# Performance work log

Measured on AMD Instinct MI355X. Metric: run time of the kernel, lower is better.

The kernel has to match this reference:

```python
import jax, jax.numpy as jnp
import numpy as np

# Standard 2D morphsnakes structuring elements (4 line filters), matching the
# repo-level global `filters` used by LSNet2.
_SE = np.zeros((4, 3, 3), dtype=np.float32)
_SE[0, 1, :] = 1.0           # horizontal line
_SE[1, :, 1] = 1.0           # vertical line
_SE[2] = np.eye(3, dtype=np.float32)          # main diagonal
_SE[3] = np.eye(3, dtype=np.float32)[::-1]    # anti-diagonal


def _dilate_stack(x, filts):
    # per-pixel: max over 3x3 window of (zero-padded x + filt), for every filter
    H, W = x.shape
    p = jnp.pad(x, 1)
    m = jnp.full((filts.shape[0], H, W), -jnp.inf, x.dtype)
    for k in range(3):
        for l in range(3):
            m = jnp.maximum(m, p[k:k + H, l:l + W][None] + filts[:, k, l][:, None, None])
    return m  # [F, H, W]


def _erode_stack(x, filts):
    # per-pixel: min over 3x3 window of (zero-padded x - filt) == -max(-(x - filt))
    H, W = x.shape
    p = jnp.pad(x, 1)
    m = jnp.full((filts.shape[0], H, W), jnp.inf, x.dtype)
    for k in range(3):
        for l in range(3):
            m = jnp.minimum(m, p[k:k + H, l:l + W][None] - filts[:, k, l][:, None, None])
    return m  # [F, H, W]


def _dilate_min(x, filts):
    return jnp.min(_dilate_stack(x, filts), axis=0)


def _erode_max(x, filts):
    return jnp.max(_erode_stack(x, filts), axis=0)


def setup_inputs() -> dict:
    key = jax.random.key(0)
    k1, k2 = jax.random.split(key)
    H = W = 2048
    inp = jax.random.uniform(k1, (H, W), dtype=jnp.float32)
    origin = jax.random.uniform(k2, (H, W), dtype=jnp.float32)
    filters = jnp.asarray(_SE)
    return {"input": inp, "origin": origin, "filters": filters}


def reference(input, origin, filters):
    x = input
    # SI o IS smoothing: dilate/min, erode/max, erode/max, dilate/min, dilate/min, erode/max
    x = _dilate_min(x, filters)
    x = _erode_max(x, filters)
    x = _erode_max(x, filters)
    x = _dilate_min(x, filters)
    x = _dilate_min(x, filters)
    x = _erode_max(x, filters)

    # balloon force with v = 1 and a flat ones(3,3) structuring element
    ones_f = jnp.ones((1, 3, 3), x.dtype)
    aux = _dilate_stack(x, ones_f)[0]
    threshold = jnp.percentile(x, 40.0)
    x = jnp.where(origin > threshold, aux, x)

    # Chan-Vese region means and update
    c0 = jnp.sum(origin * (1.0 - x)) / (jnp.sum(1.0 - x) + 1e-8)
    c1 = jnp.sum(origin * x) / (jnp.sum(x) + 1e-8)
    cv = (origin - c1) ** 2 - (origin - c0) ** 2
    x = jnp.where(cv < 0, 1.0, jnp.where(cv > 0, 0.0, x))
    return x
```

## Files before the change

kernel.cpp:

```cpp
#include <hip/hip_runtime.h>

#define HH 2048
#define WW 2048
#define NN (HH*WW)

static constexpr unsigned RANK0 = 1677721u;
static constexpr unsigned KEYLO = 0xB000u;
static constexpr unsigned KEYHI_ = 0xC000u;
static constexpr int NBINS = 4096;
static constexpr int NPART = 2048;

#define TH 32
#define TW 128
#define LR 44
#define LCP 148

static constexpr size_t OFF_CTL    = (size_t)NN * 4;
static constexpr size_t OFF_COARSE = OFF_CTL;
static constexpr size_t OFF_UNDER  = OFF_COARSE + (size_t)NBINS * 4;
static constexpr size_t OFF_OVER   = OFF_UNDER + 4;
static constexpr size_t OFF_MIDA   = OFF_OVER + 4;
static constexpr size_t OFF_MIDB   = OFF_MIDA + 1024;
static constexpr size_t OFF_H2A    = OFF_MIDB + 1024;
static constexpr size_t OFF_H2B    = OFF_H2A + 65536ull * 4;
static constexpr size_t CTL_END    = OFF_H2B + 65536ull * 4;
static constexpr size_t CTL_BYTES  = CTL_END - OFF_CTL;
static constexpr size_t OFF_PART   = CTL_END;

__device__ __forceinline__ float mx3(float a, float b, float c){ return fmaxf(fmaxf(a,b),c); }
__device__ __forceinline__ float mn3(float a, float b, float c){ return fminf(fminf(a,b),c); }

__device__ __forceinline__ unsigned keyf(float x){
  unsigned b = __float_as_uint(x);
  return (b & 0x80000000u) ? ~b : (b | 0x80000000u);
}
__device__ __forceinline__ float keyinv(unsigned k){
  unsigned b = (k & 0x80000000u) ? (k ^ 0x80000000u) : ~k;
  return __uint_as_float(b);
}

__device__ __forceinline__ unsigned excl_scan256(unsigned v, volatile unsigned* tmp, int t){
  int lane = t & 63, wv = t >> 6;
  unsigned inc = v;
  #pragma unroll
  for (int off = 1; off < 64; off <<= 1){
    unsigned u = __shfl_up(inc, off);
    if (lane >= off) inc += u;
  }
  if (lane == 63) tmp[wv] = inc;
  __syncthreads();
  unsigned wo = 0;
  #pragma unroll
  for (int w = 0; w < 4; w++) wo += (w < wv) ? tmp[w] : 0u;
  __syncthreads();
  return wo + inc - v;
}

__device__ __forceinline__ void coarse_rank(const unsigned* __restrict__ gh,
                                            const unsigned* __restrict__ under,
                                            unsigned* cres, volatile unsigned* stmp, int t){
  unsigned bins[16], loc = 0;
  #pragma unroll
  for (int i = 0; i < 16; i++){ bins[i] = gh[t*16 + i]; loc += bins[i]; }
  unsigned run = excl_scan256(loc, stmp, t) + under[0];
  #pragma unroll
  for (int i = 0; i < 16; i++){
    unsigned cc = bins[i];
    if (cc){
      if (RANK0 >= run && RANK0 - run < cc){ cres[0] = KEYLO + (unsigned)(t*16+i); cres[1] = RANK0 - run; }
      if (RANK0+1 >= run && RANK0+1 - run < cc){ cres[2] = KEYLO + (unsigned)(t*16+i); cres[3] = RANK0+1 - run; }
    }
    run += cc;
  }
  __syncthreads();
}

__device__ __forceinline__ void rank256(const unsigned* __restrict__ h, unsigned r,
                                        unsigned* res2, volatile unsigned* stmp, int t){
  unsigned c = h[t];
  unsigned ex = excl_scan256(c, stmp, t);
  if (c && r >= ex && r - ex < c){ res2[0] = (unsigned)t; res2[1] = r - ex; }
  __syncthreads();
}

__device__ __forceinline__ void loadwin6(const float* __restrict__ src, int rowbase,
                                         int cL, int cC, int cR, float w[6]){
  float4 v = *reinterpret_cast<const float4*>(&src[rowbase + cC]);
  w[0] = src[rowbase + cL];
  w[1]=v.x; w[2]=v.y; w[3]=v.z; w[4]=v.w;
  w[5] = src[rowbase + cR];
}

__device__ __forceinline__ void morph4(bool DIL,
    const float pr[6], const float cr[6], const float nr[6], float w[4]){
  #pragma unroll
  for (int i = 0; i < 4; i++){
    if (DIL){
      float Ah = mx3(cr[i],   cr[i+1], cr[i+2]);
      float Av = mx3(pr[i+1], cr[i+1], nr[i+1]);
      float Ad = mx3(pr[i],   cr[i+1], nr[i+2]);
      float Aa = mx3(pr[i+2], cr[i+1], nr[i]);
      float tm = mx3(pr[i], pr[i+1], pr[i+2]);
      float bm = mx3(nr[i], nr[i+1], nr[i+2]);
      float M9 = mx3(tm, Ah, bm);
      w[i] = fmaxf(M9, 1.0f + fminf(fminf(Ah,Av), fminf(Ad,Aa)));
    } else {
      float Bh = mn3(cr[i],   cr[i+1], cr[i+2]);
      float Bv = mn3(pr[i+1], cr[i+1], nr[i+1]);
      float Bd = mn3(pr[i],   cr[i+1], nr[i+2]);
      float Ba = mn3(pr[i+2], cr[i+1], nr[i]);
      float tm = mn3(pr[i], pr[i+1], pr[i+2]);
      float bm = mn3(nr[i], nr[i+1], nr[i+2]);
      float m9 = mn3(tm, Bh, bm);
      w[i] = fminf(m9, fmaxf(fmaxf(Bh,Bv), fmaxf(Bd,Ba)) - 1.0f);
    }
  }
}

__global__ __launch_bounds__(256)
void fused_morph_k(const float* __restrict__ in, float* __restrict__ out,
                   unsigned* __restrict__ gh, unsigned* __restrict__ under,
                   unsigned* __restrict__ over){
  __shared__ float lds[2][LR*LCP];
  const int tilec = blockIdx.x & 15;
  const int tiler = blockIdx.x >> 4;
  const int r0 = tiler*TH, c0 = tilec*TW;

  for (int idx = threadIdx.x; idx < LR*36; idx += 256){
    int lr = idx / 36, g = idx % 36;
    int gr = r0 - 6 + lr, gc = c0 - 8 + 4*g;
    float4 v = make_float4(0.f,0.f,0.f,0.f);
    if ((unsigned)gr < (unsigned)HH && (unsigned)gc < (unsigned)WW)
      v = *reinterpret_cast<const float4*>(in + (size_t)gr*WW + gc);
    *reinterpret_cast<float4*>(&lds[0][lr*LCP + 4*g]) = v;
  }
  __syncthreads();

  const int t = threadIdx.x;
  const int g = t % 36, s = t / 36;
  const bool active = (t < 252);
  const int colC = 4*g;
  const int colL = g ? 4*g - 1 : 0;
  const int colR = (g == 35) ? 143 : 4*g + 4;
  const int gcBase = c0 - 8 + 4*g;
  const bool dilf[6] = {true,false,false,true,true,false};

  #pragma unroll 1
  for (int st = 0; st < 6; st++){
    const float* src = lds[st & 1];
    float*       dst = lds[(st & 1) ^ 1];
    if (active){
      const bool DIL = dilf[st];
      float r8[8][6];
      #pragma unroll
      for (int k = 0; k < 8; k++)
        loadwin6(src, (6*s + k)*LCP, colL, colC, colR, r8[k]);
      #pragma unroll
      for (int k = 0; k < 6; k++){
        float w[4];
        morph4(DIL, r8[k], r8[k+1], r8[k+2], w);
        int gr = r0 - 6 + 6*s + 1 + k;
        if ((unsigned)gr >= (unsigned)HH){
          w[0]=w[1]=w[2]=w[3]=0.f;
        } else {
          #pragma unroll
          for (int i = 0; i < 4; i++)
            if ((unsigned)(gcBase + i) >= (unsigned)WW) w[i] = 0.f;
        }
        *reinterpret_cast<float4*>(&dst[(6*s + 1 + k)*LCP + colC]) =
            make_float4(w[0],w[1],w[2],w[3]);
      }
    }
    __syncthreads();
  }
  unsigned* lh = reinterpret_cast<unsigned*>(&lds[1][0]);
  for (int i = threadIdx.x; i < NBINS; i += 256) lh[i] = 0;
  __syncthreads();

  unsigned uc = 0, oc = 0;
  for (int idx = threadIdx.x; idx < TH*(TW/4); idx += 256){
    int row = idx >> 5, gg = idx & 31;
    float4 v = *reinterpret_cast<const float4*>(&lds[0][(row+6)*LCP + 8 + 4*gg]);
    *reinterpret_cast<float4*>(out + (size_t)(r0+row)*WW + c0 + 4*gg) = v;
    float vv[4] = {v.x, v.y, v.z, v.w};
    #pragma unroll
    for (int i = 0; i < 4; i++){
      unsigned key = keyf(vv[i]);
      unsigned hi = key >> 16;
      if (hi >= KEYLO && hi < KEYHI_) atomicAdd(&lh[hi - KEYLO], 1u);
      else if (hi < KEYLO)            uc++;
      else                            oc++;
    }
  }
  __syncthreads();
  for (int i = threadIdx.x; i < NBINS; i += 256){
    unsigned c = lh[i];
    if (c) atomicAdd(&gh[i], c);
  }
  if (uc) atomicAdd(under, uc);
  if (oc) atomicAdd(over, oc);
}

__global__ __launch_bounds__(256)
void fine2d_k(const float* __restrict__ x,
              const unsigned* __restrict__ coarse, const unsigned* __restrict__ under,
              unsigned* __restrict__ midA, unsigned* __restrict__ midB,
              unsigned* __restrict__ h2A, unsigned* __restrict__ h2B){
  __shared__ unsigned hA[256], hB[256];
  __shared__ unsigned stmp[4], cres[4];
  const int t = threadIdx.x;
  coarse_rank(coarse, under, cres, stmp, t);
  unsigned ha = cres[0], hb = cres[2];
  bool dup = (ha == hb);
  hA[t] = 0; hB[t] = 0;
  __syncthreads();
  const int nItems = NN/4;
  for (int it = blockIdx.x*blockDim.x + t; it < nItems; it += gridDim.x*blockDim.x){
    float4 v = reinterpret_cast<const float4*>(x)[it];
    float vv[4] = {v.x, v.y, v.z, v.w};
    #pragma unroll
    for (int j = 0; j < 4; j++){
      unsigned key = keyf(vv[j]);
      unsigned hi = key >> 16;
      if (hi == ha){ atomicAdd(&hA[(key>>8)&255], 1u); atomicAdd(&h2A[key & 0xFFFFu], 1u); }
      else if (hi == hb){ atomicAdd(&hB[(key>>8)&255], 1u); atomicAdd(&h2B[key & 0xFFFFu], 1u); }
    }
  }
  __syncthreads();
  if (hA[t]) atomicAdd(&midA[t], hA[t]);
  if (!dup && hB[t]) atomicAdd(&midB[t], hB[t]);
}

__device__ __forceinline__ void load6(const float* __restrict__ p, int row, int q, float r[6]){
  if (row < 0 || row >= HH){
    r[0]=r[1]=r[2]=r[3]=r[4]=r[5]=0.f;
    return;
  }
  const float* rp = p + (size_t)row * WW;
  float4 cc = *reinterpret_cast<const float4*>(rp + q);
  r[0] = (q > 0) ? rp[q-1] : 0.f;
  r[1]=cc.x; r[2]=cc.y; r[3]=cc.z; r[4]=cc.w;
  r[5] = (q+4 < WW) ? rp[q+4] : 0.f;
}

__global__ __launch_bounds__(256)
void balloon_k(const float* __restrict__ x, const float* __restrict__ orig,
               float* __restrict__ xb,
               const unsigned* __restrict__ coarse, const unsigned* __restrict__ under,
               const unsigned* __restrict__ midA, const unsigned* __restrict__ midB,
               const unsigned* __restrict__ h2A, const unsigned* __restrict__ h2B,
               double* __restrict__ part){
  __shared__ unsigned stmp[4], cres[4], mresA[2], mresB[2], lresA[2], lresB[2];
  __shared__ double red[4][3];
  const int t = threadIdx.x;

  coarse_rank(coarse, under, cres, stmp, t);
  unsigned ha = cres[0], rA = cres[1], hb = cres[2], rB = cres[3];
  bool dupHi = (ha == hb);
  rank256(midA, rA, mresA, stmp, t);
  rank256(dupHi ? midA : midB, rB, mresB, stmp, t);
  unsigned mA = mresA[0], rA2 = mresA[1], mB = mresB[0], rB2 = mresB[1];
  rank256(h2A + (size_t)mA*256, rA2, lresA, stmp, t);
  rank256((dupHi ? h2A : h2B) + (size_t)mB*256, rB2, lresB, stmp, t);
  unsigned ka = (ha << 16) | (mA << 8) | lresA[0];
  unsigned kb = (hb << 16) | (mB << 8) | lresB[0];
  double va = (double)keyinv(ka), vb = (double)keyinv(kb);
  const double FRAC = 0.4*(double)(NN-1) - (double)RANK0;
  double thr = va + (vb - va) * FRAC;

  double s0 = 0.0, s1 = 0.0, s2 = 0.0;
  const int nItems = NN/4;
  for (int it = blockIdx.x*blockDim.x + t; it < nItems; it += gridDim.x*blockDim.x){
    int i = it >> 9;
    int q = (it & 511) << 2;
    float a[6], b[6], c[6];
    load6(x, i-1, q, a);
    load6(x, i,   q, b);
    load6(x, i+1, q, c);
    float4 og = *reinterpret_cast<const float4*>(orig + (size_t)i*WW + q);
    float ov[4] = {og.x, og.y, og.z, og.w};
    float r[4];
    #pragma unroll
    for (int j = 0; j < 4; j++){
      float M9 = mx3(mx3(a[j],a[j+1],a[j+2]), mx3(b[j],b[j+1],b[j+2]), mx3(c[j],c[j+1],c[j+2]));
      float aux = 1.0f + M9;
      float nx = ((double)ov[j] > thr) ? aux : b[j+1];
      r[j] = nx;
      s0 += (double)ov[j];
      s1 += (double)nx;
      s2 += (double)ov[j] * (double)nx;
    }
    *reinterpret_cast<float4*>(xb + (size_t)i*WW + q) = make_float4(r[0],r[1],r[2],r[3]);
  }
  for (int off = 32; off > 0; off >>= 1){
    s0 += __shfl_down(s0, off);
    s1 += __shfl_down(s1, off);
    s2 += __shfl_down(s2, off);
  }
  int lane = t & 63, wv = t >> 6;
  if (lane == 0){ red[wv][0] = s0; red[wv][1] = s1; red[wv][2] = s2; }
  __syncthreads();
  if (t == 0){
    part[blockIdx.x*3+0] = red[0][0]+red[1][0]+red[2][0]+red[3][0];
    part[blockIdx.x*3+1] = red[0][1]+red[1][1]+red[2][1]+red[3][1];
    part[blockIdx.x*3+2] = red[0][2]+red[1][2]+red[2][2]+red[3][2];
  }
}

__global__ __launch_bounds__(256)
void final_k(const float* __restrict__ orig, const float* __restrict__ xb,
             const double* __restrict__ part, float* __restrict__ out){
  __shared__ double red[4][3];
  __shared__ double cc01[2];
  const int t = threadIdx.x;
  {
    double u0 = 0, u1 = 0, u2 = 0;
    for (int b = t; b < NPART; b += 256){
      u0 += part[b*3+0]; u1 += part[b*3+1]; u2 += part[b*3+2];
    }
    for (int off = 32; off > 0; off >>= 1){
      u0 += __shfl_down(u0, off);
      u1 += __shfl_down(u1, off);
      u2 += __shfl_down(u2, off);
    }
    int lane = t & 63, wv = t >> 6;
    if (lane == 0){ red[wv][0] = u0; red[wv][1] = u1; red[wv][2] = u2; }
    __syncthreads();
    if (t == 0){
      double So = red[0][0]+red[1][0]+red[2][0]+red[3][0];
      double Sx = red[0][1]+red[1][1]+red[2][1]+red[3][1];
      double Sox= red[0][2]+red[1][2]+red[2][2]+red[3][2];
      cc01[0] = (So - Sox) / ((double)NN - Sx + 1e-8);
      cc01[1] = Sox / (Sx + 1e-8);
    }
    __syncthreads();
  }
  double c0 = cc01[0], c1 = cc01[1];
  const int nItems = NN/4;
  for (int it = blockIdx.x*blockDim.x + t; it < nItems; it += gridDim.x*blockDim.x){
    float4 og = reinterpret_cast<const float4*>(orig)[it];
    float4 xv = reinterpret_cast<const float4*>(xb)[it];
    float ov[4] = {og.x, og.y, og.z, og.w};
    float xx[4] = {xv.x, xv.y, xv.z, xv.w};
    float r[4];
    #pragma unroll
    for (int j = 0; j < 4; j++){
      double o = (double)ov[j];
      double d1 = o - c1, d0 = o - c0;
      double cv = d1*d1 - d0*d0;
      r[j] = (cv < 0.0) ? 1.0f : ((cv > 0.0) ? 0.0f : xx[j]);
    }
    reinterpret_cast<float4*>(out)[it] = make_float4(r[0],r[1],r[2],r[3]);
  }
}

extern "C" void kernel_launch(void* const* d_in, const int* in_sizes, int n_in,
                              void* d_out, int out_size, void* d_ws, size_t ws_size,
                              hipStream_t stream) {
  const float* input  = (const float*)d_in[0];
  const float* origin = (const float*)d_in[1];
  float* out = (float*)d_out;

  char* ws = (char*)d_ws;
  float*    bufA   = (float*)ws;
  unsigned* coarse = (unsigned*)(ws + OFF_COARSE);
  unsigned* under  = (unsigned*)(ws + OFF_UNDER);
  unsigned* over   = (unsigned*)(ws + OFF_OVER);
  unsigned* midA   = (unsigned*)(ws + OFF_MIDA);
  unsigned* midB   = (unsigned*)(ws + OFF_MIDB);
  unsigned* h2A    = (unsigned*)(ws + OFF_H2A);
  unsigned* h2B    = (unsigned*)(ws + OFF_H2B);
  double*   part   = (double*)(ws + OFF_PART);

  hipMemsetAsync(ws + OFF_CTL, 0, CTL_BYTES, stream);

  fused_morph_k<<<(HH/TH)*(WW/TW), 256, 0, stream>>>(input, out, coarse, under, over);
  fine2d_k<<<2048, 256, 0, stream>>>(out, coarse, under, midA, midB, h2A, h2B);
  balloon_k<<<2048, 256, 0, stream>>>(out, origin, bufA, coarse, under,
                                      midA, midB, h2A, h2B, part);
  final_k<<<2048, 256, 0, stream>>>(origin, bufA, part, out);
}
```

Baseline: 124.2 us.

## Hoist c0/c1 reduction into single-block kernel, shrink grids, use float4 halo loads

Moves the partial-sum reduction and c0/c1 computation out of every final_k block into a separate one-block kernel that writes the two scalars to workspace, so final_k just reads them. The balloon grid shrinks to 512 blocks (fewer partials) and fine2d to 1024 blocks. The morph stencil loads its left and right halo values with aligned float4 LDS reads instead of scalar reads. This removes redundant reductions across 2048 blocks, at the cost of an extra kernel launch and possibly less parallelism in the resized kernels.

Result: faster. 112.7 us (median of 3 runs) (-9.3%).

```diff
diff --git a/kernel.cpp b/kernel.cpp
--- a/kernel.cpp
+++ b/kernel.cpp
@@ -8,12 +8,16 @@
 static constexpr unsigned KEYLO = 0xB000u;
 static constexpr unsigned KEYHI_ = 0xC000u;
 static constexpr int NBINS = 4096;
-static constexpr int NPART = 2048;
+static constexpr int NPART = 512;
 
 #define TH 32
 #define TW 128
 #define LR 44
 #define LCP 148
+
+struct Scal {
+  double c0, c1;
+};
 
 static constexpr size_t OFF_CTL    = (size_t)NN * 4;
 static constexpr size_t OFF_COARSE = OFF_CTL;
@@ -25,7 +29,8 @@
 static constexpr size_t OFF_H2B    = OFF_H2A + 65536ull * 4;
 static constexpr size_t CTL_END    = OFF_H2B + 65536ull * 4;
 static constexpr size_t CTL_BYTES  = CTL_END - OFF_CTL;
-static constexpr size_t OFF_PART   = CTL_END;
+static constexpr size_t OFF_SCAL   = CTL_END;
+static constexpr size_t OFF_PART   = OFF_SCAL + 64;
 
 __device__ __forceinline__ float mx3(float a, float b, float c){ return fmaxf(fmaxf(a,b),c); }
 __device__ __forceinline__ float mn3(float a, float b, float c){ return fminf(fminf(a,b),c); }
@@ -83,12 +88,14 @@
   __syncthreads();
 }
 
-__device__ __forceinline__ void loadwin6(const float* __restrict__ src, int rowbase,
-                                         int cL, int cC, int cR, float w[6]){
-  float4 v = *reinterpret_cast<const float4*>(&src[rowbase + cC]);
-  w[0] = src[rowbase + cL];
+__device__ __forceinline__ void loadwin3q(const float* __restrict__ src, int rowbase,
+                                          int gL, int gC, int gR, float w[6]){
+  float4 vp = *reinterpret_cast<const float4*>(&src[rowbase + 4*gL]);
+  float4 v  = *reinterpret_cast<const float4*>(&src[rowbase + 4*gC]);
+  float4 vn = *reinterpret_cast<const float4*>(&src[rowbase + 4*gR]);
+  w[0] = vp.w;
   w[1]=v.x; w[2]=v.y; w[3]=v.z; w[4]=v.w;
-  w[5] = src[rowbase + cR];
+  w[5] = vn.x;
 }
 
 __device__ __forceinline__ void morph4(bool DIL,
@@ -139,9 +146,8 @@
   const int t = threadIdx.x;
   const int g = t % 36, s = t / 36;
   const bool active = (t < 252);
-  const int colC = 4*g;
-  const int colL = g ? 4*g - 1 : 0;
-  const int colR = (g == 35) ? 143 : 4*g + 4;
+  const int gL = g ? g - 1 : 0;
+  const int gR = (g == 35) ? 35 : g + 1;
   const int gcBase = c0 - 8 + 4*g;
   const bool dilf[6] = {true,false,false,true,true,false};
 
@@ -154,7 +160,7 @@
       float r8[8][6];
       #pragma unroll
       for (int k = 0; k < 8; k++)
-        loadwin6(src, (6*s + k)*LCP, colL, colC, colR, r8[k]);
+        loadwin3q(src, (6*s + k)*LCP, gL, g, gR, r8[k]);
       #pragma unroll
       for (int k = 0; k < 6; k++){
         float w[4];
@@ -167,7 +173,7 @@
           for (int i = 0; i < 4; i++)
             if ((unsigned)(gcBase + i) >= (unsigned)WW) w[i] = 0.f;
         }
-        *reinterpret_cast<float4*>(&dst[(6*s + 1 + k)*LCP + colC]) =
+        *reinterpret_cast<float4*>(&dst[(6*s + 1 + k)*LCP + 4*g]) =
             make_float4(w[0],w[1],w[2],w[3]);
       }
     }
@@ -307,48 +313,47 @@
   }
 }
 
+__global__ void c0c1_k(const double* __restrict__ part, Scal* __restrict__ sc){
+  int t = threadIdx.x;
+  double s0 = 0, s1 = 0, s2 = 0;
+  for (int b = t; b < NPART; b += 256){
+    s0 += part[b*3+0]; s1 += part[b*3+1]; s2 += part[b*3+2];
+  }
+  for (int off = 32; off > 0; off >>= 1){
+    s0 += __shfl_down(s0, off);
+    s1 += __shfl_down(s1, off);
+    s2 += __shfl_down(s2, off);
+  }
+  __shared__ double red[4][3];
+  int lane = t & 63, wv = t >> 6;
+  if (lane == 0){ red[wv][0] = s0; red[wv][1] = s1; red[wv][2] = s2; }
+  __syncthreads();
+  if (t == 0){
+    double So = red[0][0]+red[1][0]+red[2][0]+red[3][0];
+    double Sx = red[0][1]+red[1][1]+red[2][1]+red[3][1];
+    double Sox= red[0][2]+red[1][2]+red[2][2]+red[3][2];
+    sc->c0 = (So - Sox) / ((double)NN - Sx + 1e-8);
+    sc->c1 = Sox / (Sx + 1e-8);
+  }
+}
+
 __global__ __launch_bounds__(256)
 void final_k(const float* __restrict__ orig, const float* __restrict__ xb,
-             const double* __restrict__ part, float* __restrict__ out){
-  __shared__ double red[4][3];
-  __shared__ double cc01[2];
-  const int t = threadIdx.x;
-  {
-    double u0 = 0, u1 = 0, u2 = 0;
-    for (int b = t; b < NPART; b += 256){
-      u0 += part[b*3+0]; u1 += part[b*3+1]; u2 += part[b*3+2];
-    }
-    for (int off = 32; off > 0; off >>= 1){
-      u0 += __shfl_down(u0, off);
-      u1 += __shfl_down(u1, off);
-      u2 += __shfl_down(u2, off);
-    }
-    int lane = t & 63, wv = t >> 6;
-    if (lane == 0){ red[wv][0] = u0; red[wv][1] = u1; red[wv][2] = u2; }
-    __syncthreads();
-    if (t == 0){
-      double So = red[0][0]+red[1][0]+red[2][0]+red[3][0];
-      double Sx = red[0][1]+red[1][1]+red[2][1]+red[3][1];
-      double Sox= red[0][2]+red[1][2]+red[2][2]+red[3][2];
-      cc01[0] = (So - Sox) / ((double)NN - Sx + 1e-8);
-      cc01[1] = Sox / (Sx + 1e-8);
-    }
-    __syncthreads();
-  }
-  double c0 = cc01[0], c1 = cc01[1];
+             const Scal* __restrict__ sc, float* __restrict__ out){
+  double c0 = sc->c0, c1 = sc->c1;
   const int nItems = NN/4;
-  for (int it = blockIdx.x*blockDim.x + t; it < nItems; it += gridDim.x*blockDim.x){
+  for (int it = blockIdx.x*blockDim.x + threadIdx.x; it < nItems; it += gridDim.x*blockDim.x){
     float4 og = reinterpret_cast<const float4*>(orig)[it];
     float4 xv = reinterpret_cast<const float4*>(xb)[it];
     float ov[4] = {og.x, og.y, og.z, og.w};
     float xx[4] = {xv.x, xv.y, xv.z, xv.w};
     float r[4];
     #pragma unroll
-    for (int j = 0; j < 4; j++){
-      double o = (double)ov[j];
+    for (int t = 0; t < 4; t++){
+      double o = (double)ov[t];
       double d1 = o - c1, d0 = o - c0;
       double cv = d1*d1 - d0*d0;
-      r[j] = (cv < 0.0) ? 1.0f : ((cv > 0.0) ? 0.0f : xx[j]);
+      r[t] = (cv < 0.0) ? 1.0f : ((cv > 0.0) ? 0.0f : xx[t]);
     }
     reinterpret_cast<float4*>(out)[it] = make_float4(r[0],r[1],r[2],r[3]);
   }
@@ -370,13 +375,15 @@
   unsigned* midB   = (unsigned*)(ws + OFF_MIDB);
   unsigned* h2A    = (unsigned*)(ws + OFF_H2A);
   unsigned* h2B    = (unsigned*)(ws + OFF_H2B);
+  Scal*     scal   = (Scal*)(ws + OFF_SCAL);
   double*   part   = (double*)(ws + OFF_PART);
 
   hipMemsetAsync(ws + OFF_CTL, 0, CTL_BYTES, stream);
 
   fused_morph_k<<<(HH/TH)*(WW/TW), 256, 0, stream>>>(input, out, coarse, under, over);
-  fine2d_k<<<2048, 256, 0, stream>>>(out, coarse, under, midA, midB, h2A, h2B);
-  balloon_k<<<2048, 256, 0, stream>>>(out, origin, bufA, coarse, under,
-                                      midA, midB, h2A, h2B, part);
-  final_k<<<2048, 256, 0, stream>>>(origin, bufA, part, out);
-}
+  fine2d_k<<<1024, 256, 0, stream>>>(out, coarse, under, midA, midB, h2A, h2B);
+  balloon_k<<<NPART, 256, 0, stream>>>(out, origin, bufA, coarse, under,
+                                       midA, midB, h2A, h2B, part);
+  c0c1_k<<<1, 256, 0, stream>>>(part, scal);
+  final_k<<<2048, 256, 0, stream>>>(origin, bufA, scal, out);
+}
```
